# Kernel tuning notes

Measured on AMD Instinct MI355X. Metric: run time of the kernel, lower is better.

The kernel has to match this reference:

```python
import jax, jax.numpy as jnp
import numpy as np

B, T, N, D = 4, 12, 512, 128
L = 4            # max_lag + 1 lag encoders
H = D // 2       # lag-encoder hidden dim
THRESHOLD = 0.1


def setup_inputs() -> dict:
    key = jax.random.key(0)
    ks = jax.random.split(key, 10)
    s = 0.02
    return {
        "x":   jax.random.normal(ks[0], (B, T, N, D), dtype=jnp.float32),
        # lag encoders: Linear(D->H), ReLU, Linear(H->D), stacked over L lags
        "W1":  s * jax.random.normal(ks[1], (L, D, H), dtype=jnp.float32),
        "b1":  jnp.zeros((L, H), dtype=jnp.float32),
        "W2":  s * jax.random.normal(ks[2], (L, H, D), dtype=jnp.float32),
        "b2":  jnp.zeros((L, D), dtype=jnp.float32),
        # causal scorer: Linear(2D->D), ReLU, (Dropout=id in eval), Linear(D->1), Sigmoid
        "Ws1": s * jax.random.normal(ks[3], (2 * D, D), dtype=jnp.float32),
        "bs1": jnp.zeros((D,), dtype=jnp.float32),
        "Ws2": s * jax.random.normal(ks[4], (D, 1), dtype=jnp.float32),
        "bs2": jnp.zeros((1,), dtype=jnp.float32),
    }


def reference(x, W1, b1, W2, b2, Ws1, bs1, Ws2, bs2):
    Tdim = x.shape[1]
    # lagged slices x[:, T-1-lag] for lag in 0..L-1 (all lags active since T > max_lag)
    lags = jnp.stack([x[:, max(0, Tdim - 1 - l)] for l in range(L)], axis=1)  # (B,L,N,D)
    h = jax.nn.relu(jnp.einsum('blnd,ldh->blnh', lags, W1) + b1[None, :, None, :])
    enc = jnp.einsum('blnh,lhd->blnd', h, W2) + b2[None, :, None, :]          # (B,L,N,D)
    agg = enc.mean(axis=1)                                                    # (B,N,D)

    # pairwise causal scorer. cat([src, tgt]) @ Ws1 == src @ Ws1[:D] + tgt @ Ws1[D:],
    # avoiding the explicit (B,N,N,2D) concat.
    src_proj = jnp.einsum('bnd,dk->bnk', agg, Ws1[:D])   # (B,N,D)
    tgt_proj = jnp.einsum('bnd,dk->bnk', agg, Ws1[D:])   # (B,N,D)
    pre = src_proj[:, :, None, :] + tgt_proj[:, None, :, :] + bs1  # (B,N,N,D)
    score = jax.nn.sigmoid(jnp.einsum('bijd,d->bij', jax.nn.relu(pre), Ws2[:, 0]) + bs2[0])

    # threshold sparsification + remove self loops
    adj = jnp.where(score > THRESHOLD, score, 0.0)
    adj = adj * (1.0 - jnp.eye(N, dtype=adj.dtype))

    # multi-hop propagation and global max normalization per batch element
    a2 = jnp.matmul(adj, adj)
    a3 = jnp.matmul(a2, adj)
    enhanced = adj + 0.5 * a2 + 0.25 * a3
    mx = jnp.max(enhanced, axis=(-1, -2), keepdims=True)
    return enhanced / (mx + 1e-8)
```

## Files before the change

kernel.cpp:

```cpp
#include <hip/hip_runtime.h>
#include <math.h>

#define Bn 4
#define Tn 12
#define Nn 512
#define Dn 128
#define Ln 4
#define Hn 64

typedef __attribute__((ext_vector_type(8))) short short8;
typedef __attribute__((ext_vector_type(4))) float f32x4;

__device__ __forceinline__ unsigned short f2bf(float f) {
    unsigned int u = __float_as_uint(f);
    unsigned int r = (u + 0x7FFF + ((u >> 16) & 1)) >> 16;
    return (unsigned short)r;
}
__device__ __forceinline__ float bf2f(unsigned short s) {
    return __uint_as_float(((unsigned int)s) << 16);
}

__global__ __launch_bounds__(256) void k_enc(
    const float* __restrict__ x,  const float* __restrict__ W1, const float* __restrict__ b1,
    const float* __restrict__ W2, const float* __restrict__ b2,
    const float* __restrict__ Ws1, const float* __restrict__ bs1,
    unsigned short* __restrict__ spb, unsigned short* __restrict__ tpb,
    unsigned int* __restrict__ maxslot)
{
    __shared__ __align__(16) unsigned char ldsraw[47616];
    unsigned short* hA   = (unsigned short*)ldsraw;
    unsigned short* wT   = (unsigned short*)(ldsraw + 8448);
    unsigned short* aggA = (unsigned short*)(ldsraw + 43264);
    unsigned short* xA   = aggA;
    int tid  = threadIdx.x;
    int bid  = blockIdx.x;
    int wv   = __builtin_amdgcn_readfirstlane(tid >> 6);
    int lane = tid & 63;
    if (bid == 0 && tid < Bn) maxslot[tid] = 0u;

    int r0 = bid * 16;
    int bb = r0 >> 9, n0 = r0 & 511;
    int m = lane & 15, q = lane >> 4;
    int colL = lane & 15, rq = lane >> 4;

    for (int lag = 0; lag < Ln; ++lag) {
        __syncthreads();
        {
            const float4* xs = (const float4*)(x + ((size_t)(bb*Tn + (Tn-1-lag))*Nn + n0)*Dn);
            for (int v = tid; v < 512; v += 256) {
                float4 f = xs[v];
                int row = v >> 5, c4 = v & 31;
                ushort4 o = { f2bf(f.x), f2bf(f.y), f2bf(f.z), f2bf(f.w) };
                *(ushort4*)&xA[row*136 + c4*4] = o;
            }
        }
        {
            int n = tid & 63, kq = tid >> 6;
            const float* Wp = W1 + (size_t)lag*Dn*Hn;
            #pragma unroll
            for (int r = 0; r < 4; ++r) {
                int k0 = (r*4 + kq)*8;
                unsigned short tmp[8];
                #pragma unroll
                for (int j = 0; j < 8; ++j) tmp[j] = f2bf(Wp[(size_t)(k0+j)*Hn + n]);
                *(short8*)&wT[n*136 + k0] = *(const short8*)tmp;
            }
        }
        __syncthreads();
        f32x4 acc = {0.f,0.f,0.f,0.f};
        #pragma unroll
        for (int ks = 0; ks < 4; ++ks) {
            short8 af = *(const short8*)&xA[m*136 + ks*32 + q*8];
            short8 bg = *(const short8*)&wT[(wv*16 + m)*136 + ks*32 + q*8];
            acc = __builtin_amdgcn_mfma_f32_16x16x32_bf16(af, bg, acc, 0, 0, 0);
        }
        int ncol = wv*16 + colL;
        float bv = b1[lag*Hn + ncol];
        #pragma unroll
        for (int reg = 0; reg < 4; ++reg)
            hA[(rq*4+reg)*264 + lag*64 + ncol] = f2bf(fmaxf(acc[reg] + bv, 0.f));
    }

    for (int ch = 0; ch < 2; ++ch) {
        __syncthreads();
        {
            int n = tid & 63, kq = tid >> 6;
            #pragma unroll
            for (int r = 0; r < 8; ++r) {
                int k0 = (r*4 + kq)*8;
                unsigned short tmp[8];
                #pragma unroll
                for (int j = 0; j < 8; ++j) tmp[j] = f2bf(W2[(size_t)(k0+j)*Dn + ch*64 + n]);
                *(short8*)&wT[n*264 + k0] = *(const short8*)tmp;
            }
        }
        __syncthreads();
        f32x4 acc = {0.f,0.f,0.f,0.f};
        #pragma unroll
        for (int ks = 0; ks < 8; ++ks) {
            short8 af = *(const short8*)&hA[m*264 + ks*32 + q*8];
            short8 bg = *(const short8*)&wT[(wv*16 + m)*264 + ks*32 + q*8];
            acc = __builtin_amdgcn_mfma_f32_16x16x32_bf16(af, bg, acc, 0, 0, 0);
        }
        int col = ch*64 + wv*16 + colL;
        float b2s = b2[col] + b2[Dn+col] + b2[2*Dn+col] + b2[3*Dn+col];
        #pragma unroll
        for (int reg = 0; reg < 4; ++reg)
            aggA[(rq*4+reg)*136 + col] = f2bf(0.25f*(acc[reg] + b2s));
    }

    for (int tgt = 0; tgt < 2; ++tgt) {
        __syncthreads();
        {
            int n = tid & 127, kq = tid >> 7;
            #pragma unroll
            for (int r = 0; r < 8; ++r) {
                int k0 = (r*2 + kq)*8;
                unsigned short tmp[8];
                #pragma unroll
                for (int j = 0; j < 8; ++j)
                    tmp[j] = f2bf(Ws1[(size_t)(tgt*Dn + k0 + j)*Dn + n]);
                *(short8*)&wT[n*136 + k0] = *(const short8*)tmp;
            }
        }
        __syncthreads();
        f32x4 acc[2] = {{0.f,0.f,0.f,0.f},{0.f,0.f,0.f,0.f}};
        #pragma unroll
        for (int ks = 0; ks < 4; ++ks) {
            short8 af = *(const short8*)&aggA[m*136 + ks*32 + q*8];
            #pragma unroll
            for (int nt = 0; nt < 2; ++nt) {
                short8 bg = *(const short8*)&wT[(wv*32 + nt*16 + m)*136 + ks*32 + q*8];
                acc[nt] = __builtin_amdgcn_mfma_f32_16x16x32_bf16(af, bg, acc[nt], 0, 0, 0);
            }
        }
        unsigned short* dst = tgt ? tpb : spb;
        #pragma unroll
        for (int nt = 0; nt < 2; ++nt) {
            int n = wv*32 + nt*16 + colL;
            float bv = tgt ? 0.f : bs1[n];
            #pragma unroll
            for (int reg = 0; reg < 4; ++reg)
                dst[(size_t)(r0 + rq*4 + reg)*Dn + n] = f2bf(acc[nt][reg] + bv);
        }
    }
}

__global__ __launch_bounds__(256) void k_score(
    const unsigned short* __restrict__ spb, const unsigned short* __restrict__ tpb,
    const float* __restrict__ Ws2, const float* __restrict__ bs2,
    unsigned short* __restrict__ adj_b, unsigned short* __restrict__ adj_bt)
{
    __shared__ float spl[64*132];
    __shared__ unsigned short tplT[Dn*72];
    int tid = threadIdx.x;
    int wv = __builtin_amdgcn_readfirstlane(tid >> 6);
    int lane = tid & 63;
    int bz = blockIdx.z;
    int i0b = blockIdx.y * 64, j0b = blockIdx.x * 64;
    const unsigned short* spr = spb + (size_t)bz*Nn*Dn;
    const unsigned short* tpr = tpb + (size_t)bz*Nn*Dn;

    for (int v = tid; v < 1024; v += 256) {
        int row = v >> 4, c = v & 15;
        const unsigned short* src = spr + (size_t)(i0b+row)*Dn + c*8;
        ushort4 u0 = *(const ushort4*)src;
        ushort4 u1 = *(const ushort4*)(src + 4);
        float4 f0 = { bf2f(u0.x), bf2f(u0.y), bf2f(u0.z), bf2f(u0.w) };
        float4 f1 = { bf2f(u1.x), bf2f(u1.y), bf2f(u1.z), bf2f(u1.w) };
        *(float4*)&spl[row*132 + c*8]     = f0;
        *(float4*)&spl[row*132 + c*8 + 4] = f1;
    }
    {
        int j = tid & 63, kq = tid >> 6;
        for (int p = 0; p < 4; ++p) {
            int k8 = p*4 + kq;
            short8 tv = *(const short8*)(tpr + (size_t)(j0b+j)*Dn + k8*8);
            #pragma unroll
            for (int t = 0; t < 8; ++t) tplT[(k8*8+t)*72 + j] = (unsigned short)tv[t];
        }
    }
    __syncthreads();

    int iq = lane >> 4, jq = lane & 15;
    int iw = wv*16 + iq*4;
    float acc[4][4] = {};
    for (int k8 = 0; k8 < 16; ++k8) {
        float4 wa = *(const float4*)(Ws2 + k8*8);
        float4 wb = *(const float4*)(Ws2 + k8*8 + 4);
        float4 sA[4], sB[4];
        #pragma unroll
        for (int ii = 0; ii < 4; ++ii) {
            sA[ii] = *(const float4*)&spl[(iw+ii)*132 + k8*8];
            sB[ii] = *(const float4*)&spl[(iw+ii)*132 + k8*8 + 4];
        }
        ushort4 t4[8];
        #pragma unroll
        for (int kk = 0; kk < 8; ++kk) t4[kk] = *(const ushort4*)&tplT[(k8*8+kk)*72 + jq*4];
        #pragma unroll
        for (int kk = 0; kk < 8; ++kk) {
            float w = (kk < 4) ? ((const float*)&wa)[kk] : ((const float*)&wb)[kk-4];
            float tv0 = bf2f(t4[kk].x), tv1 = bf2f(t4[kk].y);
            float tv2 = bf2f(t4[kk].z), tv3 = bf2f(t4[kk].w);
            #pragma unroll
            for (int ii = 0; ii < 4; ++ii) {
                float s = (kk < 4) ? ((const float*)&sA[ii])[kk] : ((const float*)&sB[ii])[kk-4];
                acc[ii][0] += fmaxf(s + tv0, 0.f)*w;
                acc[ii][1] += fmaxf(s + tv1, 0.f)*w;
                acc[ii][2] += fmaxf(s + tv2, 0.f)*w;
                acc[ii][3] += fmaxf(s + tv3, 0.f)*w;
            }
        }
    }
    float bsv = bs2[0];
    int i0 = i0b + iw;
    int j0 = j0b + jq*4;
    float vals[4][4];
    #pragma unroll
    for (int ii = 0; ii < 4; ++ii) {
        int i = i0 + ii;
        #pragma unroll
        for (int jj = 0; jj < 4; ++jj) {
            float z = acc[ii][jj] + bsv;
            float sc = 1.f/(1.f + __expf(-z));
            int j = j0 + jj;
            vals[ii][jj] = (sc > 0.1f && i != j) ? sc : 0.f;
        }
    }
    size_t base = (size_t)bz << 18;
    #pragma unroll
    for (int ii = 0; ii < 4; ++ii) {
        ushort4 rv = make_ushort4(f2bf(vals[ii][0]), f2bf(vals[ii][1]),
                                  f2bf(vals[ii][2]), f2bf(vals[ii][3]));
        *(ushort4*)(adj_b + base + (size_t)(i0+ii)*Nn + j0) = rv;
    }
    #pragma unroll
    for (int jj = 0; jj < 4; ++jj) {
        ushort4 cv = make_ushort4(f2bf(vals[0][jj]), f2bf(vals[1][jj]),
                                  f2bf(vals[2][jj]), f2bf(vals[3][jj]));
        *(ushort4*)(adj_bt + base + (size_t)(j0+jj)*Nn + i0) = cv;
    }
}

__global__ __launch_bounds__(256) void k_mm1(
    const unsigned short* __restrict__ adj_b, const unsigned short* __restrict__ adj_bt,
    unsigned short* __restrict__ a2b)
{
    __shared__ unsigned short Als[64*72];
    __shared__ unsigned short Bls[64*72];
    int tid = threadIdx.x;
    int wv = __builtin_amdgcn_readfirstlane(tid >> 6);
    int lane = tid & 63;
    int b = blockIdx.z, i0 = blockIdx.y*64, j0 = blockIdx.x*64;
    size_t base = (size_t)b << 18;
    const unsigned short* Ab = adj_b + base;
    const unsigned short* Bb = adj_bt + base;
    int wm = wv >> 1, wn = wv & 1;
    int m = lane & 15, q = lane >> 4;
    int sr = tid >> 2, sc = (tid & 3)*16;
    f32x4 acc[2][2];
    #pragma unroll
    for (int mt = 0; mt < 2; ++mt)
        #pragma unroll
        for (int nt = 0; nt < 2; ++nt) acc[mt][nt] = (f32x4){0.f,0.f,0.f,0.f};
    short8 pa0, pa1, pb0, pb1;
    pa0 = *(const short8*)(Ab + (size_t)(i0+sr)*Nn + sc);
    pa1 = *(const short8*)(Ab + (size_t)(i0+sr)*Nn + sc + 8);
    pb0 = *(const short8*)(Bb + (size_t)(j0+sr)*Nn + sc);
    pb1 = *(const short8*)(Bb + (size_t)(j0+sr)*Nn + sc + 8);
    for (int kt = 0; kt < 8; ++kt) {
        *(short8*)&Als[sr*72 + sc]     = pa0;
        *(short8*)&Als[sr*72 + sc + 8] = pa1;
        *(short8*)&Bls[sr*72 + sc]     = pb0;
        *(short8*)&Bls[sr*72 + sc + 8] = pb1;
        __syncthreads();
        if (kt < 7) {
            int k0 = (kt+1)*64;
            pa0 = *(const short8*)(Ab + (size_t)(i0+sr)*Nn + k0 + sc);
            pa1 = *(const short8*)(Ab + (size_t)(i0+sr)*Nn + k0 + sc + 8);
            pb0 = *(const short8*)(Bb + (size_t)(j0+sr)*Nn + k0 + sc);
            pb1 = *(const short8*)(Bb + (size_t)(j0+sr)*Nn + k0 + sc + 8);
        }
        #pragma unroll
        for (int ks = 0; ks < 2; ++ks) {
            short8 af[2], bg[2];
            #pragma unroll
            for (int mt = 0; mt < 2; ++mt) af[mt] = *(const short8*)&Als[(wm*32+mt*16+m)*72 + ks*32 + q*8];
            #pragma unroll
            for (int nt = 0; nt < 2; ++nt) bg[nt] = *(const short8*)&Bls[(wn*32+nt*16+m)*72 + ks*32 + q*8];
            #pragma unroll
            for (int mt = 0; mt < 2; ++mt)
                #pragma unroll
                for (int nt = 0; nt < 2; ++nt)
                    acc[mt][nt] = __builtin_amdgcn_mfma_f32_16x16x32_bf16(af[mt], bg[nt], acc[mt][nt], 0, 0, 0);
        }
        __syncthreads();
    }
    int col = lane & 15, rq = lane >> 4;
    #pragma unroll
    for (int mt = 0; mt < 2; ++mt)
        #pragma unroll
        for (int nt = 0; nt < 2; ++nt)
            #pragma unroll
            for (int reg = 0; reg < 4; ++reg) {
                int i = i0 + wm*32 + mt*16 + rq*4 + reg;
                int j = j0 + wn*32 + nt*16 + col;
                a2b[base + (size_t)i*Nn + j] = f2bf(acc[mt][nt][reg]);
            }
}

__global__ __launch_bounds__(256) void k_mm2(
    const unsigned short* __restrict__ adj_b, const unsigned short* __restrict__ adj_bt,
    const unsigned short* __restrict__ a2b,
    float* __restrict__ out, unsigned int* __restrict__ maxslot)
{
    __shared__ unsigned short Als[64*72];
    __shared__ unsigned short Bls[64*72];
    __shared__ float red[4];
    int tid = threadIdx.x;
    int wv = __builtin_amdgcn_readfirstlane(tid >> 6);
    int lane = tid & 63;
    int b = blockIdx.z, i0 = blockIdx.y*64, j0 = blockIdx.x*64;
    size_t base = (size_t)b << 18;
    const unsigned short* Ab = a2b + base;
    const unsigned short* Bb = adj_bt + base;
    int wm = wv >> 1, wn = wv & 1;
    int m = lane & 15, q = lane >> 4;
    int sr = tid >> 2, sc = (tid & 3)*16;
    f32x4 acc[2][2];
    #pragma unroll
    for (int mt = 0; mt < 2; ++mt)
        #pragma unroll
        for (int nt = 0; nt < 2; ++nt) acc[mt][nt] = (f32x4){0.f,0.f,0.f,0.f};
    short8 pa0, pa1, pb0, pb1;
    pa0 = *(const short8*)(Ab + (size_t)(i0+sr)*Nn + sc);
    pa1 = *(const short8*)(Ab + (size_t)(i0+sr)*Nn + sc + 8);
    pb0 = *(const short8*)(Bb + (size_t)(j0+sr)*Nn + sc);
    pb1 = *(const short8*)(Bb + (size_t)(j0+sr)*Nn + sc + 8);
    for (int kt = 0; kt < 8; ++kt) {
        *(short8*)&Als[sr*72 + sc]     = pa0;
        *(short8*)&Als[sr*72 + sc + 8] = pa1;
        *(short8*)&Bls[sr*72 + sc]     = pb0;
        *(short8*)&Bls[sr*72 + sc + 8] = pb1;
        __syncthreads();
        if (kt < 7) {
            int k0 = (kt+1)*64;
            pa0 = *(const short8*)(Ab + (size_t)(i0+sr)*Nn + k0 + sc);
            pa1 = *(const short8*)(Ab + (size_t)(i0+sr)*Nn + k0 + sc + 8);
            pb0 = *(const short8*)(Bb + (size_t)(j0+sr)*Nn + k0 + sc);
            pb1 = *(const short8*)(Bb + (size_t)(j0+sr)*Nn + k0 + sc + 8);
        }
        #pragma unroll
        for (int ks = 0; ks < 2; ++ks) {
            short8 af[2], bg[2];
            #pragma unroll
            for (int mt = 0; mt < 2; ++mt) af[mt] = *(const short8*)&Als[(wm*32+mt*16+m)*72 + ks*32 + q*8];
            #pragma unroll
            for (int nt = 0; nt < 2; ++nt) bg[nt] = *(const short8*)&Bls[(wn*32+nt*16+m)*72 + ks*32 + q*8];
            #pragma unroll
            for (int mt = 0; mt < 2; ++mt)
                #pragma unroll
                for (int nt = 0; nt < 2; ++nt)
                    acc[mt][nt] = __builtin_amdgcn_mfma_f32_16x16x32_bf16(af[mt], bg[nt], acc[mt][nt], 0, 0, 0);
        }
        __syncthreads();
    }
    int col = lane & 15, rq = lane >> 4;
    float lmax = 0.f;
    const unsigned short* adjp = adj_b + base;
    #pragma unroll
    for (int mt = 0; mt < 2; ++mt)
        #pragma unroll
        for (int nt = 0; nt < 2; ++nt)
            #pragma unroll
            for (int reg = 0; reg < 4; ++reg) {
                int i = i0 + wm*32 + mt*16 + rq*4 + reg;
                int j = j0 + wn*32 + nt*16 + col;
                size_t off = (size_t)i*Nn + j;
                float e = bf2f(adjp[off]) + 0.5f*bf2f(Ab[off]) + 0.25f*acc[mt][nt][reg];
                out[base + off] = e;
                lmax = fmaxf(lmax, e);
            }
    #pragma unroll
    for (int s = 1; s < 64; s <<= 1) lmax = fmaxf(lmax, __shfl_xor(lmax, s, 64));
    if (lane == 0) red[wv] = lmax;
    __syncthreads();
    if (tid == 0) {
        float mx = fmaxf(fmaxf(red[0], red[1]), fmaxf(red[2], red[3]));
        atomicMax(maxslot + b, __float_as_uint(mx));
    }
}

__global__ __launch_bounds__(256) void k_norm(float* __restrict__ out,
                                              const unsigned int* __restrict__ maxslot)
{
    int idx = blockIdx.x*256 + threadIdx.x;
    int b = idx >> 16;
    float m = __uint_as_float(maxslot[b]);
    float inv = 1.f/(m + 1e-8f);
    float4* p = (float4*)out + idx;
    float4 v = *p;
    v.x *= inv; v.y *= inv; v.z *= inv; v.w *= inv;
    *p = v;
}

extern "C" void kernel_launch(void* const* d_in, const int* in_sizes, int n_in,
                              void* d_out, int out_size, void* d_ws, size_t ws_size,
                              hipStream_t stream) {
    const float* x   = (const float*)d_in[0];
    const float* W1  = (const float*)d_in[1];
    const float* b1  = (const float*)d_in[2];
    const float* W2  = (const float*)d_in[3];
    const float* b2  = (const float*)d_in[4];
    const float* Ws1 = (const float*)d_in[5];
    const float* bs1 = (const float*)d_in[6];
    const float* Ws2 = (const float*)d_in[7];
    const float* bs2 = (const float*)d_in[8];
    float* out = (float*)d_out;

    unsigned char* wsb = (unsigned char*)d_ws;
    unsigned short* spb    = (unsigned short*)(wsb);
    unsigned short* tpb    = (unsigned short*)(wsb + (512u<<10));
    unsigned short* adj_b  = (unsigned short*)(wsb + (1024u<<10));
    unsigned short* adj_bt = (unsigned short*)(wsb + (3072u<<10));
    unsigned short* a2b    = (unsigned short*)(wsb + (5120u<<10));
    unsigned int*   maxslot= (unsigned int*)(wsb + (7168u<<10));

    k_enc  <<<dim3(128),      256, 0, stream>>>(x, W1, b1, W2, b2, Ws1, bs1, spb, tpb, maxslot);
    k_score<<<dim3(8, 8, Bn), 256, 0, stream>>>(spb, tpb, Ws2, bs2, adj_b, adj_bt);
    k_mm1  <<<dim3(8, 8, Bn), 256, 0, stream>>>(adj_b, adj_bt, a2b);
    k_mm2  <<<dim3(8, 8, Bn), 256, 0, stream>>>(adj_b, adj_bt, a2b, out, maxslot);
    k_norm <<<dim3(1024),     256, 0, stream>>>(out, maxslot);
}
```

Before: 126.0 us.

## Pre-pack bf16 weights once and use packed fp16 dot2 in pairwise scorer

A new k_prep kernel converts and transposes W1, W2 and Ws1 to bf16 once per call. k_enc then reads these packed weights directly from global memory instead of re-converting them into LDS in every block, which also removes several barriers. The projections are now stored as fp16, and the scorer inner loop uses packed half add/max followed by fdot2 accumulation, cutting ALU work per pair roughly in half. This adds one more launch and introduces fp16 rounding in the relu-sum before the threshold, which may move scores near the cutoff.

After: 118.6 us. -5.8%, faster.

```diff
diff --git a/kernel.cpp b/kernel.cpp
--- a/kernel.cpp
+++ b/kernel.cpp
@@ -10,6 +10,7 @@
 
 typedef __attribute__((ext_vector_type(8))) short short8;
 typedef __attribute__((ext_vector_type(4))) float f32x4;
+typedef _Float16 h2 __attribute__((ext_vector_type(2)));
 
 __device__ __forceinline__ unsigned short f2bf(float f) {
     unsigned int u = __float_as_uint(f);
@@ -19,19 +20,58 @@
 __device__ __forceinline__ float bf2f(unsigned short s) {
     return __uint_as_float(((unsigned int)s) << 16);
 }
+__device__ __forceinline__ float fdot2(h2 a, h2 b, float c) {
+#if defined(__has_builtin)
+#if __has_builtin(__builtin_amdgcn_fdot2)
+    return __builtin_amdgcn_fdot2(a, b, c, false);
+#else
+    return c + (float)a.x*(float)b.x + (float)a.y*(float)b.y;
+#endif
+#else
+    return c + (float)a.x*(float)b.x + (float)a.y*(float)b.y;
+#endif
+}
+
+__global__ __launch_bounds__(256) void k_prep(
+    const float* __restrict__ W1, const float* __restrict__ W2, const float* __restrict__ Ws1,
+    unsigned short* __restrict__ w1p, unsigned short* __restrict__ w2p,
+    unsigned short* __restrict__ wsp)
+{
+    int g = blockIdx.x*256 + threadIdx.x;
+    unsigned short tmp[8];
+    if (g < 4096) {
+        int lag = g >> 10, r = g & 1023;
+        int n = r >> 4, k8 = r & 15;
+        #pragma unroll
+        for (int j = 0; j < 8; ++j) tmp[j] = f2bf(W1[(size_t)(lag*128 + k8*8 + j)*64 + n]);
+        *(short8*)(w1p + (size_t)lag*8192 + n*128 + k8*8) = *(const short8*)tmp;
+    } else if (g < 8192) {
+        int r = g - 4096;
+        int n = r >> 5, k8 = r & 31;
+        #pragma unroll
+        for (int j = 0; j < 8; ++j) tmp[j] = f2bf(W2[(size_t)(k8*8 + j)*128 + n]);
+        *(short8*)(w2p + (size_t)n*256 + k8*8) = *(const short8*)tmp;
+    } else {
+        int r = g - 8192;
+        int tgt = r >> 11, r2 = r & 2047;
+        int n = r2 >> 4, k8 = r2 & 15;
+        #pragma unroll
+        for (int j = 0; j < 8; ++j) tmp[j] = f2bf(Ws1[(size_t)(tgt*128 + k8*8 + j)*128 + n]);
+        *(short8*)(wsp + (size_t)tgt*16384 + n*128 + k8*8) = *(const short8*)tmp;
+    }
+}
 
 __global__ __launch_bounds__(256) void k_enc(
-    const float* __restrict__ x,  const float* __restrict__ W1, const float* __restrict__ b1,
-    const float* __restrict__ W2, const float* __restrict__ b2,
-    const float* __restrict__ Ws1, const float* __restrict__ bs1,
+    const float* __restrict__ x,  const float* __restrict__ b1,
+    const float* __restrict__ b2, const float* __restrict__ bs1,
+    const unsigned short* __restrict__ w1p, const unsigned short* __restrict__ w2p,
+    const unsigned short* __restrict__ wsp,
     unsigned short* __restrict__ spb, unsigned short* __restrict__ tpb,
     unsigned int* __restrict__ maxslot)
 {
-    __shared__ __align__(16) unsigned char ldsraw[47616];
-    unsigned short* hA   = (unsigned short*)ldsraw;
-    unsigned short* wT   = (unsigned short*)(ldsraw + 8448);
-    unsigned short* aggA = (unsigned short*)(ldsraw + 43264);
-    unsigned short* xA   = aggA;
+    __shared__ __align__(16) unsigned short hA[16*264];
+    __shared__ __align__(16) unsigned short xA[16*136];
+    __shared__ __align__(16) unsigned short aggA[16*136];
     int tid  = threadIdx.x;
     int bid  = blockIdx.x;
     int wv   = __builtin_amdgcn_readfirstlane(tid >> 6);
@@ -54,24 +94,12 @@
                 *(ushort4*)&xA[row*136 + c4*4] = o;
             }
         }
-        {
-            int n = tid & 63, kq = tid >> 6;
-            const float* Wp = W1 + (size_t)lag*Dn*Hn;
-            #pragma unroll
-            for (int r = 0; r < 4; ++r) {
-                int k0 = (r*4 + kq)*8;
-                unsigned short tmp[8];
-                #pragma unroll
-                for (int j = 0; j < 8; ++j) tmp[j] = f2bf(Wp[(size_t)(k0+j)*Hn + n]);
-                *(short8*)&wT[n*136 + k0] = *(const short8*)tmp;
-            }
-        }
         __syncthreads();
         f32x4 acc = {0.f,0.f,0.f,0.f};
         #pragma unroll
         for (int ks = 0; ks < 4; ++ks) {
             short8 af = *(const short8*)&xA[m*136 + ks*32 + q*8];
-            short8 bg = *(const short8*)&wT[(wv*16 + m)*136 + ks*32 + q*8];
+            short8 bg = *(const short8*)(w1p + (size_t)lag*8192 + (wv*16+m)*128 + ks*32 + q*8);
             acc = __builtin_amdgcn_mfma_f32_16x16x32_bf16(af, bg, acc, 0, 0, 0);
         }
         int ncol = wv*16 + colL;
@@ -80,26 +108,15 @@
         for (int reg = 0; reg < 4; ++reg)
             hA[(rq*4+reg)*264 + lag*64 + ncol] = f2bf(fmaxf(acc[reg] + bv, 0.f));
     }
-
+    __syncthreads();
+
+    #pragma unroll
     for (int ch = 0; ch < 2; ++ch) {
-        __syncthreads();
-        {
-            int n = tid & 63, kq = tid >> 6;
-            #pragma unroll
-            for (int r = 0; r < 8; ++r) {
-                int k0 = (r*4 + kq)*8;
-                unsigned short tmp[8];
-                #pragma unroll
-                for (int j = 0; j < 8; ++j) tmp[j] = f2bf(W2[(size_t)(k0+j)*Dn + ch*64 + n]);
-                *(short8*)&wT[n*264 + k0] = *(const short8*)tmp;
-            }
-        }
-        __syncthreads();
         f32x4 acc = {0.f,0.f,0.f,0.f};
         #pragma unroll
         for (int ks = 0; ks < 8; ++ks) {
             short8 af = *(const short8*)&hA[m*264 + ks*32 + q*8];
-            short8 bg = *(const short8*)&wT[(wv*16 + m)*264 + ks*32 + q*8];
+            short8 bg = *(const short8*)(w2p + (size_t)(ch*64 + wv*16 + m)*256 + ks*32 + q*8);
             acc = __builtin_amdgcn_mfma_f32_16x16x32_bf16(af, bg, acc, 0, 0, 0);
         }
         int col = ch*64 + wv*16 + colL;
@@ -108,29 +125,17 @@
         for (int reg = 0; reg < 4; ++reg)
             aggA[(rq*4+reg)*136 + col] = f2bf(0.25f*(acc[reg] + b2s));
     }
-
+    __syncthreads();
+
+    #pragma unroll
     for (int tgt = 0; tgt < 2; ++tgt) {
-        __syncthreads();
-        {
-            int n = tid & 127, kq = tid >> 7;
-            #pragma unroll
-            for (int r = 0; r < 8; ++r) {
-                int k0 = (r*2 + kq)*8;
-                unsigned short tmp[8];
-                #pragma unroll
-                for (int j = 0; j < 8; ++j)
-                    tmp[j] = f2bf(Ws1[(size_t)(tgt*Dn + k0 + j)*Dn + n]);
-                *(short8*)&wT[n*136 + k0] = *(const short8*)tmp;
-            }
-        }
-        __syncthreads();
         f32x4 acc[2] = {{0.f,0.f,0.f,0.f},{0.f,0.f,0.f,0.f}};
         #pragma unroll
         for (int ks = 0; ks < 4; ++ks) {
             short8 af = *(const short8*)&aggA[m*136 + ks*32 + q*8];
             #pragma unroll
             for (int nt = 0; nt < 2; ++nt) {
-                short8 bg = *(const short8*)&wT[(wv*32 + nt*16 + m)*136 + ks*32 + q*8];
+                short8 bg = *(const short8*)(wsp + (size_t)tgt*16384 + (wv*32 + nt*16 + m)*128 + ks*32 + q*8);
                 acc[nt] = __builtin_amdgcn_mfma_f32_16x16x32_bf16(af, bg, acc[nt], 0, 0, 0);
             }
         }
@@ -140,8 +145,10 @@
             int n = wv*32 + nt*16 + colL;
             float bv = tgt ? 0.f : bs1[n];
             #pragma unroll
-            for (int reg = 0; reg < 4; ++reg)
-                dst[(size_t)(r0 + rq*4 + reg)*Dn + n] = f2bf(acc[nt][reg] + bv);
+            for (int reg = 0; reg < 4; ++reg) {
+                _Float16 hv = (_Float16)(acc[nt][reg] + bv);
+                dst[(size_t)(r0 + rq*4 + reg)*Dn + n] = __builtin_bit_cast(unsigned short, hv);
+            }
         }
     }
 }
@@ -151,8 +158,9 @@
     const float* __restrict__ Ws2, const float* __restrict__ bs2,
     unsigned short* __restrict__ adj_b, unsigned short* __restrict__ adj_bt)
 {
-    __shared__ float spl[64*132];
-    __shared__ unsigned short tplT[Dn*72];
+    __shared__ unsigned int spl[64*65];
+    __shared__ unsigned int tpl[64*65];
+    __shared__ unsigned int wl[64];
     int tid = threadIdx.x;
     int wv = __builtin_amdgcn_readfirstlane(tid >> 6);
     int lane = tid & 63;
@@ -163,54 +171,37 @@
 
     for (int v = tid; v < 1024; v += 256) {
         int row = v >> 4, c = v & 15;
-        const unsigned short* src = spr + (size_t)(i0b+row)*Dn + c*8;
-        ushort4 u0 = *(const ushort4*)src;
-        ushort4 u1 = *(const ushort4*)(src + 4);
-        float4 f0 = { bf2f(u0.x), bf2f(u0.y), bf2f(u0.z), bf2f(u0.w) };
-        float4 f1 = { bf2f(u1.x), bf2f(u1.y), bf2f(u1.z), bf2f(u1.w) };
-        *(float4*)&spl[row*132 + c*8]     = f0;
-        *(float4*)&spl[row*132 + c*8 + 4] = f1;
-    }
-    {
-        int j = tid & 63, kq = tid >> 6;
-        for (int p = 0; p < 4; ++p) {
-            int k8 = p*4 + kq;
-            short8 tv = *(const short8*)(tpr + (size_t)(j0b+j)*Dn + k8*8);
-            #pragma unroll
-            for (int t = 0; t < 8; ++t) tplT[(k8*8+t)*72 + j] = (unsigned short)tv[t];
-        }
+        uint4 gs = *(const uint4*)(spr + (size_t)(i0b+row)*Dn + c*8);
+        uint4 gt = *(const uint4*)(tpr + (size_t)(j0b+row)*Dn + c*8);
+        spl[row*65 + c*4 + 0] = gs.x; spl[row*65 + c*4 + 1] = gs.y;
+        spl[row*65 + c*4 + 2] = gs.z; spl[row*65 + c*4 + 3] = gs.w;
+        tpl[row*65 + c*4 + 0] = gt.x; tpl[row*65 + c*4 + 1] = gt.y;
+        tpl[row*65 + c*4 + 2] = gt.z; tpl[row*65 + c*4 + 3] = gt.w;
+    }
+    if (tid < 64) {
+        h2 hw = { (_Float16)Ws2[tid*2], (_Float16)Ws2[tid*2+1] };
+        wl[tid] = __builtin_bit_cast(unsigned int, hw);
     }
     __syncthreads();
 
     int iq = lane >> 4, jq = lane & 15;
     int iw = wv*16 + iq*4;
     float acc[4][4] = {};
-    for (int k8 = 0; k8 < 16; ++k8) {
-        float4 wa = *(const float4*)(Ws2 + k8*8);
-        float4 wb = *(const float4*)(Ws2 + k8*8 + 4);
-        float4 sA[4], sB[4];
-        #pragma unroll
-        for (int ii = 0; ii < 4; ++ii) {
-            sA[ii] = *(const float4*)&spl[(iw+ii)*132 + k8*8];
-            sB[ii] = *(const float4*)&spl[(iw+ii)*132 + k8*8 + 4];
-        }
-        ushort4 t4[8];
-        #pragma unroll
-        for (int kk = 0; kk < 8; ++kk) t4[kk] = *(const ushort4*)&tplT[(k8*8+kk)*72 + jq*4];
-        #pragma unroll
-        for (int kk = 0; kk < 8; ++kk) {
-            float w = (kk < 4) ? ((const float*)&wa)[kk] : ((const float*)&wb)[kk-4];
-            float tv0 = bf2f(t4[kk].x), tv1 = bf2f(t4[kk].y);
-            float tv2 = bf2f(t4[kk].z), tv3 = bf2f(t4[kk].w);
-            #pragma unroll
-            for (int ii = 0; ii < 4; ++ii) {
-                float s = (kk < 4) ? ((const float*)&sA[ii])[kk] : ((const float*)&sB[ii])[kk-4];
-                acc[ii][0] += fmaxf(s + tv0, 0.f)*w;
-                acc[ii][1] += fmaxf(s + tv1, 0.f)*w;
-                acc[ii][2] += fmaxf(s + tv2, 0.f)*w;
-                acc[ii][3] += fmaxf(s + tv3, 0.f)*w;
-            }
-        }
+    #pragma unroll 4
+    for (int c = 0; c < 64; ++c) {
+        h2 wp = __builtin_bit_cast(h2, wl[c]);
+        h2 sh[4], th[4];
+        #pragma unroll
+        for (int ii = 0; ii < 4; ++ii) sh[ii] = __builtin_bit_cast(h2, spl[(iw+ii)*65 + c]);
+        #pragma unroll
+        for (int jj = 0; jj < 4; ++jj) th[jj] = __builtin_bit_cast(h2, tpl[(jq*4+jj)*65 + c]);
+        #pragma unroll
+        for (int ii = 0; ii < 4; ++ii)
+            #pragma unroll
+            for (int jj = 0; jj < 4; ++jj) {
+                h2 r = __builtin_elementwise_max(sh[ii] + th[jj], (h2){(_Float16)0.f,(_Float16)0.f});
+                acc[ii][jj] = fdot2(r, wp, acc[ii][jj]);
+            }
     }
     float bsv = bs2[0];
     int i0 = i0b + iw;
@@ -425,8 +416,12 @@
     unsigned short* adj_bt = (unsigned short*)(wsb + (3072u<<10));
     unsigned short* a2b    = (unsigned short*)(wsb + (5120u<<10));
     unsigned int*   maxslot= (unsigned int*)(wsb + (7168u<<10));
-
-    k_enc  <<<dim3(128),      256, 0, stream>>>(x, W1, b1, W2, b2, Ws1, bs1, spb, tpb, maxslot);
+    unsigned short* w1p    = (unsigned short*)(wsb + (7172u<<10));
+    unsigned short* w2p    = (unsigned short*)(wsb + (7236u<<10));
+    unsigned short* wsp    = (unsigned short*)(wsb + (7300u<<10));
+
+    k_prep <<<dim3(48),       256, 0, stream>>>(W1, W2, Ws1, w1p, w2p, wsp);
+    k_enc  <<<dim3(128),      256, 0, stream>>>(x, b1, b2, bs1, w1p, w2p, wsp, spb, tpb, maxslot);
     k_score<<<dim3(8, 8, Bn), 256, 0, stream>>>(spb, tpb, Ws2, bs2, adj_b, adj_bt);
     k_mm1  <<<dim3(8, 8, Bn), 256, 0, stream>>>(adj_b, adj_bt, a2b);
     k_mm2  <<<dim3(8, 8, Bn), 256, 0, stream>>>(adj_b, adj_bt, a2b, out, maxslot);
```
